# Performance work log

Measured on AMD Instinct MI355X. Metric: run time of the kernel, lower is better.

Reference implementation:

```python
import jax, jax.numpy as jnp
import numpy as np

N = 10000   # nodes
E = 320000  # edges
F = 512     # input features
H1 = 32
H2 = 16


def setup_inputs() -> dict:
    key = jax.random.key(0)
    k1, k2, k3, k4, k5, k6 = jax.random.split(key, 6)
    x = jax.random.normal(k1, (N, F), dtype=jnp.float32)
    edge_row = jax.random.randint(k2, (E,), 0, N, dtype=jnp.int32)
    edge_col = jax.random.randint(k3, (E,), 0, N, dtype=jnp.int32)
    edge_w = jax.random.uniform(k4, (E,), dtype=jnp.float32)  # normalized adj values
    W1 = jax.random.normal(k5, (F, H1), dtype=jnp.float32) * (1.0 / np.sqrt(F))
    W2 = jax.random.normal(k6, (H1, H2), dtype=jnp.float32) * (1.0 / np.sqrt(H1))
    return {"x": x, "edge_w": edge_w, "W1": W1, "W2": W2,
            "edge_row": edge_row, "edge_col": edge_col}


def _spmm(edge_w, edge_row, edge_col, h):
    # sparse A @ h : gather source rows, scale by edge weight, scatter-add to dest
    return jax.ops.segment_sum(edge_w[:, None] * h[edge_col], edge_row, num_segments=N)


def reference(x, edge_w, W1, W2, edge_row, edge_col):
    # GCN layer 1: relu(A @ (X W1))   (dropout rate 0 -> identity)
    h1 = jax.nn.relu(_spmm(edge_w, edge_row, edge_col, x @ W1))
    # GCN layer 2 (linear act): Z = A @ (H1 W2)
    z = _spmm(edge_w, edge_row, edge_col, h1 @ W2)
    # InnerProductDecoder: flatten(Z @ Z^T)
    recon = (z @ z.T).reshape(-1)
    return recon
```

## Files before the change

### kernel.cpp

```cpp
#include <hip/hip_runtime.h>


constexpr int N_   = 10000;
constexpr int E_   = 320000;
constexpr int F_   = 512;
constexpr int H1_  = 32;
constexpr int H2_  = 16;
constexpr int CAP_ = 96;

constexpr int GEMM_BLOCKS = (N_ * H1_) / 256;
constexpr int ZERO_BLOCKS = (N_ + 255) / 256;

__global__ __launch_bounds__(256) void gemm_xw1_zero(const float* __restrict__ x,
                                                     const float* __restrict__ W1,
                                                     float* __restrict__ h,
                                                     int* __restrict__ cursor) {
    if (blockIdx.x >= GEMM_BLOCKS) {
        int i = (blockIdx.x - GEMM_BLOCKS) * 256 + threadIdx.x;
        if (i < N_) cursor[i] = 0;
        return;
    }
    int tid = blockIdx.x * blockDim.x + threadIdx.x;
    int r = tid >> 5;
    int c = tid & (H1_ - 1);
    const float4* xr = reinterpret_cast<const float4*>(x + (size_t)r * F_);
    float acc = 0.f;
#pragma unroll 8
    for (int k4 = 0; k4 < F_ / 4; ++k4) {
        float4 xv = xr[k4];
        int k = k4 * 4;
        acc = fmaf(xv.x, W1[(k + 0) * H1_ + c], acc);
        acc = fmaf(xv.y, W1[(k + 1) * H1_ + c], acc);
        acc = fmaf(xv.z, W1[(k + 2) * H1_ + c], acc);
        acc = fmaf(xv.w, W1[(k + 3) * H1_ + c], acc);
    }
    h[tid] = acc;
}

__global__ __launch_bounds__(256) void scatter_ell(const int* __restrict__ erow,
                                                   const int* __restrict__ ecol,
                                                   const float* __restrict__ ew,
                                                   int* __restrict__ cursor,
                                                   int* __restrict__ cole,
                                                   float* __restrict__ we) {
    int e = blockIdx.x * blockDim.x + threadIdx.x;
    if (e >= E_) return;
    int r = erow[e];
    int p = atomicAdd(&cursor[r], 1);
    if (p < CAP_) {
        size_t idx = (size_t)r * CAP_ + p;
        cole[idx] = ecol[e];
        we[idx]   = ew[e];
    }
}

__global__ __launch_bounds__(256) void spmm1_mlp(const float* __restrict__ h,
                                                 const int* __restrict__ cursor,
                                                 const int* __restrict__ cole,
                                                 const float* __restrict__ we,
                                                 const float* __restrict__ W2,
                                                 float* __restrict__ h2) {
    __shared__ float sh1[8][H1_ + 1];
    __shared__ float sW2[H1_ * H2_];
    const int t = threadIdx.x;
    sW2[t]       = W2[t];
    sW2[t + 256] = W2[t + 256];

    const int rl = t >> 5;
    const int f  = t & (H1_ - 1);
    const int r  = blockIdx.x * 8 + rl;
    float acc = 0.f;
    if (r < N_) {
        const int deg = cursor[r];
        const int*   cp = cole + (size_t)r * CAP_;
        const float* wp = we   + (size_t)r * CAP_;
        int p = 0;
        for (; p + 4 <= deg; p += 4) {
            int c0 = cp[p], c1 = cp[p + 1], c2 = cp[p + 2], c3 = cp[p + 3];
            float w0 = wp[p], w1 = wp[p + 1], w2v = wp[p + 2], w3 = wp[p + 3];
            float g0 = h[(size_t)c0 * H1_ + f];
            float g1 = h[(size_t)c1 * H1_ + f];
            float g2 = h[(size_t)c2 * H1_ + f];
            float g3 = h[(size_t)c3 * H1_ + f];
            acc = fmaf(w0, g0, acc);
            acc = fmaf(w1, g1, acc);
            acc = fmaf(w2v, g2, acc);
            acc = fmaf(w3, g3, acc);
        }
        for (; p < deg; ++p)
            acc = fmaf(wp[p], h[(size_t)cp[p] * H1_ + f], acc);
    }
    sh1[rl][f] = fmaxf(acc, 0.f);
    __syncthreads();

    if (t < 128) {
        const int r2l = t >> 4;
        const int c   = t & (H2_ - 1);
        const int r2  = blockIdx.x * 8 + r2l;
        if (r2 < N_) {
            float a = 0.f;
#pragma unroll
            for (int k = 0; k < H1_; ++k)
                a = fmaf(sh1[r2l][k], sW2[k * H2_ + c], a);
            h2[(size_t)r2 * H2_ + c] = a;
        }
    }
}

__global__ __launch_bounds__(256) void spmm2(const float* __restrict__ h2,
                                             const int* __restrict__ cursor,
                                             const int* __restrict__ cole,
                                             const float* __restrict__ we,
                                             float* __restrict__ z) {
    const int t = threadIdx.x;
    const int rl = t >> 4;
    const int f  = t & (H2_ - 1);
    const int r  = blockIdx.x * 16 + rl;
    if (r >= N_) return;
    const int deg = cursor[r];
    const int*   cp = cole + (size_t)r * CAP_;
    const float* wp = we   + (size_t)r * CAP_;
    float acc = 0.f;
    int p = 0;
    for (; p + 4 <= deg; p += 4) {
        int c0 = cp[p], c1 = cp[p + 1], c2 = cp[p + 2], c3 = cp[p + 3];
        float w0 = wp[p], w1 = wp[p + 1], w2v = wp[p + 2], w3 = wp[p + 3];
        float g0 = h2[(size_t)c0 * H2_ + f];
        float g1 = h2[(size_t)c1 * H2_ + f];
        float g2 = h2[(size_t)c2 * H2_ + f];
        float g3 = h2[(size_t)c3 * H2_ + f];
        acc = fmaf(w0, g0, acc);
        acc = fmaf(w1, g1, acc);
        acc = fmaf(w2v, g2, acc);
        acc = fmaf(w3, g3, acc);
    }
    for (; p < deg; ++p)
        acc = fmaf(wp[p], h2[(size_t)cp[p] * H2_ + f], acc);
    z[(size_t)r * H2_ + f] = acc;
}

constexpr int BI = 32;
constexpr int BJ = 128;

__global__ __launch_bounds__(256) void zzt(const float* __restrict__ z,
                                           float* __restrict__ out) {
    __shared__ float zi[H2_][BI + 4];
    __shared__ float zj[H2_][BJ + 4];
    const int t  = threadIdx.x;
    const int ib = blockIdx.y * BI;
    const int jb = blockIdx.x * BJ;

    for (int idx = t; idx < BI * H2_; idx += 256) {
        int rl = idx >> 4;
        int k  = idx & 15;
        int gr = ib + rl;
        zi[k][rl] = (gr < N_) ? z[(size_t)gr * H2_ + k] : 0.f;
    }
    for (int idx = t; idx < BJ * H2_; idx += 256) {
        int rl = idx >> 4;
        int k  = idx & 15;
        int gr = jb + rl;
        zj[k][rl] = (gr < N_) ? z[(size_t)gr * H2_ + k] : 0.f;
    }
    __syncthreads();

    const int il = (t >> 5) << 2;
    const int jl = (t & 31) << 2;

    float acc[4][4] = {};
#pragma unroll
    for (int k = 0; k < H2_; ++k) {
        float4 a = *reinterpret_cast<const float4*>(&zi[k][il]);
        float4 b = *reinterpret_cast<const float4*>(&zj[k][jl]);
        acc[0][0] = fmaf(a.x, b.x, acc[0][0]);
        acc[0][1] = fmaf(a.x, b.y, acc[0][1]);
        acc[0][2] = fmaf(a.x, b.z, acc[0][2]);
        acc[0][3] = fmaf(a.x, b.w, acc[0][3]);
        acc[1][0] = fmaf(a.y, b.x, acc[1][0]);
        acc[1][1] = fmaf(a.y, b.y, acc[1][1]);
        acc[1][2] = fmaf(a.y, b.z, acc[1][2]);
        acc[1][3] = fmaf(a.y, b.w, acc[1][3]);
        acc[2][0] = fmaf(a.z, b.x, acc[2][0]);
        acc[2][1] = fmaf(a.z, b.y, acc[2][1]);
        acc[2][2] = fmaf(a.z, b.z, acc[2][2]);
        acc[2][3] = fmaf(a.z, b.w, acc[2][3]);
        acc[3][0] = fmaf(a.w, b.x, acc[3][0]);
        acc[3][1] = fmaf(a.w, b.y, acc[3][1]);
        acc[3][2] = fmaf(a.w, b.z, acc[3][2]);
        acc[3][3] = fmaf(a.w, b.w, acc[3][3]);
    }

#pragma unroll
    for (int ii = 0; ii < 4; ++ii) {
        int gi = ib + il + ii;
        if (gi >= N_) continue;
        int gj = jb + jl;
        float* orow = out + (size_t)gi * N_ + gj;
        if (gj + 3 < N_) {
            *reinterpret_cast<float4*>(orow) =
                make_float4(acc[ii][0], acc[ii][1], acc[ii][2], acc[ii][3]);
        } else {
#pragma unroll
            for (int jj = 0; jj < 4; ++jj)
                if (gj + jj < N_) orow[jj] = acc[ii][jj];
        }
    }
}

extern "C" void kernel_launch(void* const* d_in, const int* in_sizes, int n_in,
                              void* d_out, int out_size, void* d_ws, size_t ws_size,
                              hipStream_t stream) {
    const float* x    = (const float*)d_in[0];
    const float* ew   = (const float*)d_in[1];
    const float* W1   = (const float*)d_in[2];
    const float* W2   = (const float*)d_in[3];
    const int*   erow = (const int*)d_in[4];
    const int*   ecol = (const int*)d_in[5];
    float* out = (float*)d_out;

    float* h      = (float*)d_ws;
    float* h2     = h  + (size_t)N_ * H1_;
    float* z      = h2 + (size_t)N_ * H2_;
    float* we     = z  + (size_t)N_ * H2_;
    int*   cole   = (int*)(we + (size_t)N_ * CAP_);
    int*   cursor = cole + (size_t)N_ * CAP_;

    gemm_xw1_zero<<<GEMM_BLOCKS + ZERO_BLOCKS, 256, 0, stream>>>(x, W1, h, cursor);
    scatter_ell<<<(E_ + 255) / 256, 256, 0, stream>>>(erow, ecol, ew, cursor, cole, we);
    spmm1_mlp<<<(N_ + 7) / 8, 256, 0, stream>>>(h, cursor, cole, we, W2, h2);
    spmm2<<<(N_ + 15) / 16, 256, 0, stream>>>(h2, cursor, cole, we, z);

    dim3 grid((N_ + BJ - 1) / BJ, (N_ + BI - 1) / BI);
    zzt<<<grid, 256, 0, stream>>>(z, out);
}
```

Measured before the change: 216.1 us.

## Make ZZ^T blocks persistent over quarter-row strips, reusing the i-tile

```diff
diff --git a/kernel.cpp b/kernel.cpp
--- a/kernel.cpp
+++ b/kernel.cpp
@@ -139,70 +139,74 @@
     z[(size_t)r * H2_ + f] = acc;
 }
 
-constexpr int BI = 32;
-constexpr int BJ = 128;
-
-__global__ __launch_bounds__(256) void zzt(const float* __restrict__ z,
-                                           float* __restrict__ out) {
-    __shared__ float zi[H2_][BI + 4];
-    __shared__ float zj[H2_][BJ + 4];
+constexpr int ZBI = 32;
+constexpr int ZBJ = 128;
+constexpr int NQ  = 4;
+constexpr int QW  = N_ / NQ;
+constexpr int NSTRIP = (N_ + ZBI - 1) / ZBI;
+
+__global__ __launch_bounds__(256) void zzt_strip(const float* __restrict__ z,
+                                                 float* __restrict__ out) {
+    __shared__ float zi[H2_][ZBI + 4];
+    __shared__ float zj[H2_][ZBJ + 4];
     const int t  = threadIdx.x;
-    const int ib = blockIdx.y * BI;
-    const int jb = blockIdx.x * BJ;
-
-    for (int idx = t; idx < BI * H2_; idx += 256) {
-        int rl = idx >> 4;
-        int k  = idx & 15;
+    const int ib = (blockIdx.x >> 2) * ZBI;
+    const int jq = (blockIdx.x & 3) * QW;
+
+    for (int idx = t; idx < ZBI * H2_; idx += 256) {
+        int rl = idx >> 4, k = idx & 15;
         int gr = ib + rl;
         zi[k][rl] = (gr < N_) ? z[(size_t)gr * H2_ + k] : 0.f;
     }
-    for (int idx = t; idx < BJ * H2_; idx += 256) {
-        int rl = idx >> 4;
-        int k  = idx & 15;
-        int gr = jb + rl;
-        zj[k][rl] = (gr < N_) ? z[(size_t)gr * H2_ + k] : 0.f;
-    }
-    __syncthreads();
 
     const int il = (t >> 5) << 2;
     const int jl = (t & 31) << 2;
 
-    float acc[4][4] = {};
-#pragma unroll
-    for (int k = 0; k < H2_; ++k) {
-        float4 a = *reinterpret_cast<const float4*>(&zi[k][il]);
-        float4 b = *reinterpret_cast<const float4*>(&zj[k][jl]);
-        acc[0][0] = fmaf(a.x, b.x, acc[0][0]);
-        acc[0][1] = fmaf(a.x, b.y, acc[0][1]);
-        acc[0][2] = fmaf(a.x, b.z, acc[0][2]);
-        acc[0][3] = fmaf(a.x, b.w, acc[0][3]);
-        acc[1][0] = fmaf(a.y, b.x, acc[1][0]);
-        acc[1][1] = fmaf(a.y, b.y, acc[1][1]);
-        acc[1][2] = fmaf(a.y, b.z, acc[1][2]);
-        acc[1][3] = fmaf(a.y, b.w, acc[1][3]);
-        acc[2][0] = fmaf(a.z, b.x, acc[2][0]);
-        acc[2][1] = fmaf(a.z, b.y, acc[2][1]);
-        acc[2][2] = fmaf(a.z, b.z, acc[2][2]);
-        acc[2][3] = fmaf(a.z, b.w, acc[2][3]);
-        acc[3][0] = fmaf(a.w, b.x, acc[3][0]);
-        acc[3][1] = fmaf(a.w, b.y, acc[3][1]);
-        acc[3][2] = fmaf(a.w, b.z, acc[3][2]);
-        acc[3][3] = fmaf(a.w, b.w, acc[3][3]);
-    }
-
-#pragma unroll
-    for (int ii = 0; ii < 4; ++ii) {
-        int gi = ib + il + ii;
-        if (gi >= N_) continue;
-        int gj = jb + jl;
-        float* orow = out + (size_t)gi * N_ + gj;
-        if (gj + 3 < N_) {
-            *reinterpret_cast<float4*>(orow) =
-                make_float4(acc[ii][0], acc[ii][1], acc[ii][2], acc[ii][3]);
-        } else {
-#pragma unroll
-            for (int jj = 0; jj < 4; ++jj)
-                if (gj + jj < N_) orow[jj] = acc[ii][jj];
+    for (int cb = 0; cb < QW; cb += ZBJ) {
+        const int w = (QW - cb < ZBJ) ? (QW - cb) : ZBJ;
+        __syncthreads();
+        for (int idx = t; idx < ZBJ * H2_; idx += 256) {
+            int rl = idx >> 4, k = idx & 15;
+            zj[k][rl] = (rl < w) ? z[(size_t)(jq + cb + rl) * H2_ + k] : 0.f;
+        }
+        __syncthreads();
+
+        float acc[4][4] = {};
+#pragma unroll
+        for (int k = 0; k < H2_; ++k) {
+            float4 a = *reinterpret_cast<const float4*>(&zi[k][il]);
+            float4 b = *reinterpret_cast<const float4*>(&zj[k][jl]);
+            acc[0][0] = fmaf(a.x, b.x, acc[0][0]);
+            acc[0][1] = fmaf(a.x, b.y, acc[0][1]);
+            acc[0][2] = fmaf(a.x, b.z, acc[0][2]);
+            acc[0][3] = fmaf(a.x, b.w, acc[0][3]);
+            acc[1][0] = fmaf(a.y, b.x, acc[1][0]);
+            acc[1][1] = fmaf(a.y, b.y, acc[1][1]);
+            acc[1][2] = fmaf(a.y, b.z, acc[1][2]);
+            acc[1][3] = fmaf(a.y, b.w, acc[1][3]);
+            acc[2][0] = fmaf(a.z, b.x, acc[2][0]);
+            acc[2][1] = fmaf(a.z, b.y, acc[2][1]);
+            acc[2][2] = fmaf(a.z, b.z, acc[2][2]);
+            acc[2][3] = fmaf(a.z, b.w, acc[2][3]);
+            acc[3][0] = fmaf(a.w, b.x, acc[3][0]);
+            acc[3][1] = fmaf(a.w, b.y, acc[3][1]);
+            acc[3][2] = fmaf(a.w, b.z, acc[3][2]);
+            acc[3][3] = fmaf(a.w, b.w, acc[3][3]);
+        }
+
+        const int gjb = jq + cb + jl;
+#pragma unroll
+        for (int ii = 0; ii < 4; ++ii) {
+            int gi = ib + il + ii;
+            if (gi >= N_) continue;
+            if (jl + 3 < w) {
+                *reinterpret_cast<float4*>(out + (size_t)gi * N_ + gjb) =
+                    make_float4(acc[ii][0], acc[ii][1], acc[ii][2], acc[ii][3]);
+            } else {
+#pragma unroll
+                for (int jj = 0; jj < 4; ++jj)
+                    if (jl + jj < w) out[(size_t)gi * N_ + gjb + jj] = acc[ii][jj];
+            }
         }
     }
 }
@@ -230,6 +234,5 @@
     spmm1_mlp<<<(N_ + 7) / 8, 256, 0, stream>>>(h, cursor, cole, we, W2, h2);
     spmm2<<<(N_ + 15) / 16, 256, 0, stream>>>(h2, cursor, cole, we, z);
 
-    dim3 grid((N_ + BJ - 1) / BJ, (N_ + BI - 1) / BI);
-    zzt<<<grid, 256, 0, stream>>>(z, out);
-}
+    zzt_strip<<<NSTRIP * NQ, 256, 0, stream>>>(z, out);
+}
```

Result: slower. 288.4 us (+33.5%).

## Fuse front GCN stages into one cooperative kernel with grid syncs

Applied to the files above, without the earlier changes.

```diff
diff --git a/kernel.cpp b/kernel.cpp
--- a/kernel.cpp
+++ b/kernel.cpp
@@ -1,4 +1,7 @@
 #include <hip/hip_runtime.h>
+#include <hip/hip_cooperative_groups.h>
+
+namespace cg = cooperative_groups;
 
 
 constexpr int N_   = 10000;
@@ -8,135 +11,132 @@
 constexpr int H2_  = 16;
 constexpr int CAP_ = 96;
 
-constexpr int GEMM_BLOCKS = (N_ * H1_) / 256;
-constexpr int ZERO_BLOCKS = (N_ + 255) / 256;
-
-__global__ __launch_bounds__(256) void gemm_xw1_zero(const float* __restrict__ x,
-                                                     const float* __restrict__ W1,
-                                                     float* __restrict__ h,
-                                                     int* __restrict__ cursor) {
-    if (blockIdx.x >= GEMM_BLOCKS) {
-        int i = (blockIdx.x - GEMM_BLOCKS) * 256 + threadIdx.x;
-        if (i < N_) cursor[i] = 0;
-        return;
-    }
-    int tid = blockIdx.x * blockDim.x + threadIdx.x;
-    int r = tid >> 5;
-    int c = tid & (H1_ - 1);
-    const float4* xr = reinterpret_cast<const float4*>(x + (size_t)r * F_);
-    float acc = 0.f;
-#pragma unroll 8
-    for (int k4 = 0; k4 < F_ / 4; ++k4) {
-        float4 xv = xr[k4];
-        int k = k4 * 4;
-        acc = fmaf(xv.x, W1[(k + 0) * H1_ + c], acc);
-        acc = fmaf(xv.y, W1[(k + 1) * H1_ + c], acc);
-        acc = fmaf(xv.z, W1[(k + 2) * H1_ + c], acc);
-        acc = fmaf(xv.w, W1[(k + 3) * H1_ + c], acc);
-    }
-    h[tid] = acc;
-}
-
-__global__ __launch_bounds__(256) void scatter_ell(const int* __restrict__ erow,
+constexpr int COOP_BLOCKS = 1024;
+
+__global__ __launch_bounds__(256) void fused_front(const float* __restrict__ x,
+                                                   const float* __restrict__ W1,
+                                                   const float* __restrict__ W2,
+                                                   const float* __restrict__ ew,
+                                                   const int* __restrict__ erow,
                                                    const int* __restrict__ ecol,
-                                                   const float* __restrict__ ew,
+                                                   float* __restrict__ h,
+                                                   float* __restrict__ h2,
+                                                   float* __restrict__ z,
                                                    int* __restrict__ cursor,
                                                    int* __restrict__ cole,
                                                    float* __restrict__ we) {
-    int e = blockIdx.x * blockDim.x + threadIdx.x;
-    if (e >= E_) return;
-    int r = erow[e];
-    int p = atomicAdd(&cursor[r], 1);
-    if (p < CAP_) {
-        size_t idx = (size_t)r * CAP_ + p;
-        cole[idx] = ecol[e];
-        we[idx]   = ew[e];
-    }
-}
-
-__global__ __launch_bounds__(256) void spmm1_mlp(const float* __restrict__ h,
-                                                 const int* __restrict__ cursor,
-                                                 const int* __restrict__ cole,
-                                                 const float* __restrict__ we,
-                                                 const float* __restrict__ W2,
-                                                 float* __restrict__ h2) {
+    cg::grid_group grid = cg::this_grid();
+    const int t     = threadIdx.x;
+    const int gtid  = blockIdx.x * 256 + t;
+    const int gsize = gridDim.x * 256;
+
+    for (int i = gtid; i < N_; i += gsize) cursor[i] = 0;
+    for (int tid = gtid; tid < N_ * H1_; tid += gsize) {
+        int r = tid >> 5;
+        int c = tid & (H1_ - 1);
+        const float4* xr = reinterpret_cast<const float4*>(x + (size_t)r * F_);
+        float acc = 0.f;
+#pragma unroll 8
+        for (int k4 = 0; k4 < F_ / 4; ++k4) {
+            float4 xv = xr[k4];
+            int k = k4 * 4;
+            acc = fmaf(xv.x, W1[(k + 0) * H1_ + c], acc);
+            acc = fmaf(xv.y, W1[(k + 1) * H1_ + c], acc);
+            acc = fmaf(xv.z, W1[(k + 2) * H1_ + c], acc);
+            acc = fmaf(xv.w, W1[(k + 3) * H1_ + c], acc);
+        }
+        h[tid] = acc;
+    }
+    grid.sync();
+
+    for (int e = gtid; e < E_; e += gsize) {
+        int r = erow[e];
+        int p = atomicAdd(&cursor[r], 1);
+        if (p < CAP_) {
+            size_t idx = (size_t)r * CAP_ + p;
+            cole[idx] = ecol[e];
+            we[idx]   = ew[e];
+        }
+    }
+    grid.sync();
+
     __shared__ float sh1[8][H1_ + 1];
     __shared__ float sW2[H1_ * H2_];
-    const int t = threadIdx.x;
     sW2[t]       = W2[t];
     sW2[t + 256] = W2[t + 256];
-
-    const int rl = t >> 5;
-    const int f  = t & (H1_ - 1);
-    const int r  = blockIdx.x * 8 + rl;
-    float acc = 0.f;
-    if (r < N_) {
+    __syncthreads();
+
+    constexpr int NGROUP1 = (N_ + 7) / 8;
+    for (int g = blockIdx.x; g < NGROUP1; g += gridDim.x) {
+        __syncthreads();
+        const int rl = t >> 5;
+        const int f  = t & (H1_ - 1);
+        const int r  = g * 8 + rl;
+        float acc = 0.f;
+        if (r < N_) {
+            const int deg = cursor[r];
+            const int*   cp = cole + (size_t)r * CAP_;
+            const float* wp = we   + (size_t)r * CAP_;
+            int p = 0;
+            for (; p + 4 <= deg; p += 4) {
+                int c0 = cp[p], c1 = cp[p + 1], c2 = cp[p + 2], c3 = cp[p + 3];
+                float w0 = wp[p], w1 = wp[p + 1], w2v = wp[p + 2], w3 = wp[p + 3];
+                float g0 = h[(size_t)c0 * H1_ + f];
+                float g1 = h[(size_t)c1 * H1_ + f];
+                float g2 = h[(size_t)c2 * H1_ + f];
+                float g3 = h[(size_t)c3 * H1_ + f];
+                acc = fmaf(w0, g0, acc);
+                acc = fmaf(w1, g1, acc);
+                acc = fmaf(w2v, g2, acc);
+                acc = fmaf(w3, g3, acc);
+            }
+            for (; p < deg; ++p)
+                acc = fmaf(wp[p], h[(size_t)cp[p] * H1_ + f], acc);
+        }
+        sh1[rl][f] = fmaxf(acc, 0.f);
+        __syncthreads();
+        if (t < 128) {
+            const int r2l = t >> 4;
+            const int c   = t & (H2_ - 1);
+            const int r2  = g * 8 + r2l;
+            if (r2 < N_) {
+                float a = 0.f;
+#pragma unroll
+                for (int k = 0; k < H1_; ++k)
+                    a = fmaf(sh1[r2l][k], sW2[k * H2_ + c], a);
+                h2[(size_t)r2 * H2_ + c] = a;
+            }
+        }
+    }
+    grid.sync();
+
+    constexpr int NGROUP2 = (N_ + 15) / 16;
+    for (int g = blockIdx.x; g < NGROUP2; g += gridDim.x) {
+        const int rl = t >> 4;
+        const int f  = t & (H2_ - 1);
+        const int r  = g * 16 + rl;
+        if (r >= N_) continue;
         const int deg = cursor[r];
         const int*   cp = cole + (size_t)r * CAP_;
         const float* wp = we   + (size_t)r * CAP_;
+        float acc = 0.f;
         int p = 0;
         for (; p + 4 <= deg; p += 4) {
             int c0 = cp[p], c1 = cp[p + 1], c2 = cp[p + 2], c3 = cp[p + 3];
             float w0 = wp[p], w1 = wp[p + 1], w2v = wp[p + 2], w3 = wp[p + 3];
-            float g0 = h[(size_t)c0 * H1_ + f];
-            float g1 = h[(size_t)c1 * H1_ + f];
-            float g2 = h[(size_t)c2 * H1_ + f];
-            float g3 = h[(size_t)c3 * H1_ + f];
+            float g0 = h2[(size_t)c0 * H2_ + f];
+            float g1 = h2[(size_t)c1 * H2_ + f];
+            float g2 = h2[(size_t)c2 * H2_ + f];
+            float g3 = h2[(size_t)c3 * H2_ + f];
             acc = fmaf(w0, g0, acc);
             acc = fmaf(w1, g1, acc);
             acc = fmaf(w2v, g2, acc);
             acc = fmaf(w3, g3, acc);
         }
         for (; p < deg; ++p)
-            acc = fmaf(wp[p], h[(size_t)cp[p] * H1_ + f], acc);
-    }
-    sh1[rl][f] = fmaxf(acc, 0.f);
-    __syncthreads();
-
-    if (t < 128) {
-        const int r2l = t >> 4;
-        const int c   = t & (H2_ - 1);
-        const int r2  = blockIdx.x * 8 + r2l;
-        if (r2 < N_) {
-            float a = 0.f;
-#pragma unroll
-            for (int k = 0; k < H1_; ++k)
-                a = fmaf(sh1[r2l][k], sW2[k * H2_ + c], a);
-            h2[(size_t)r2 * H2_ + c] = a;
-        }
-    }
-}
-
-__global__ __launch_bounds__(256) void spmm2(const float* __restrict__ h2,
-                                             const int* __restrict__ cursor,
-                                             const int* __restrict__ cole,
-                                             const float* __restrict__ we,
-                                             float* __restrict__ z) {
-    const int t = threadIdx.x;
-    const int rl = t >> 4;
-    const int f  = t & (H2_ - 1);
-    const int r  = blockIdx.x * 16 + rl;
-    if (r >= N_) return;
-    const int deg = cursor[r];
-    const int*   cp = cole + (size_t)r * CAP_;
-    const float* wp = we   + (size_t)r * CAP_;
-    float acc = 0.f;
-    int p = 0;
-    for (; p + 4 <= deg; p += 4) {
-        int c0 = cp[p], c1 = cp[p + 1], c2 = cp[p + 2], c3 = cp[p + 3];
-        float w0 = wp[p], w1 = wp[p + 1], w2v = wp[p + 2], w3 = wp[p + 3];
-        float g0 = h2[(size_t)c0 * H2_ + f];
-        float g1 = h2[(size_t)c1 * H2_ + f];
-        float g2 = h2[(size_t)c2 * H2_ + f];
-        float g3 = h2[(size_t)c3 * H2_ + f];
-        acc = fmaf(w0, g0, acc);
-        acc = fmaf(w1, g1, acc);
-        acc = fmaf(w2v, g2, acc);
-        acc = fmaf(w3, g3, acc);
-    }
-    for (; p < deg; ++p)
-        acc = fmaf(wp[p], h2[(size_t)cp[p] * H2_ + f], acc);
-    z[(size_t)r * H2_ + f] = acc;
+            acc = fmaf(wp[p], h2[(size_t)cp[p] * H2_ + f], acc);
+        z[(size_t)r * H2_ + f] = acc;
+    }
 }
 
 constexpr int BI = 32;
@@ -225,10 +225,12 @@
     int*   cole   = (int*)(we + (size_t)N_ * CAP_);
     int*   cursor = cole + (size_t)N_ * CAP_;
 
-    gemm_xw1_zero<<<GEMM_BLOCKS + ZERO_BLOCKS, 256, 0, stream>>>(x, W1, h, cursor);
-    scatter_ell<<<(E_ + 255) / 256, 256, 0, stream>>>(erow, ecol, ew, cursor, cole, we);
-    spmm1_mlp<<<(N_ + 7) / 8, 256, 0, stream>>>(h, cursor, cole, we, W2, h2);
-    spmm2<<<(N_ + 15) / 16, 256, 0, stream>>>(h2, cursor, cole, we, z);
+    void* args[] = {(void*)&x, (void*)&W1, (void*)&W2, (void*)&ew,
+                    (void*)&erow, (void*)&ecol,
+                    (void*)&h, (void*)&h2, (void*)&z,
+                    (void*)&cursor, (void*)&cole, (void*)&we};
+    hipLaunchCooperativeKernel((const void*)fused_front, dim3(COOP_BLOCKS),
+                               dim3(256), args, 0, stream);
 
     dim3 grid((N_ + BJ - 1) / BJ, (N_ + BI - 1) / BI);
     zzt<<<grid, 256, 0, stream>>>(z, out);
```

Result: slower. 588.3 us (+172.2%).

## Enlarge ZZ^T tiles to 64x256, vectorize staging loads, use nontemporal output stores

Applied to the files above, without the earlier changes.

```diff
diff --git a/kernel.cpp b/kernel.cpp
--- a/kernel.cpp
+++ b/kernel.cpp
@@ -7,6 +7,8 @@
 constexpr int H1_  = 32;
 constexpr int H2_  = 16;
 constexpr int CAP_ = 96;
+
+typedef float f32x4 __attribute__((ext_vector_type(4)));
 
 constexpr int GEMM_BLOCKS = (N_ * H1_) / 256;
 constexpr int ZERO_BLOCKS = (N_ + 255) / 256;
@@ -139,70 +141,93 @@
     z[(size_t)r * H2_ + f] = acc;
 }
 
-constexpr int BI = 32;
-constexpr int BJ = 128;
+constexpr int BI = 64;
+constexpr int BJ = 256;
 
 __global__ __launch_bounds__(256) void zzt(const float* __restrict__ z,
                                            float* __restrict__ out) {
     __shared__ float zi[H2_][BI + 4];
-    __shared__ float zj[H2_][BJ + 4];
+    __shared__ float zj[H2_][BJ + 8];
     const int t  = threadIdx.x;
     const int ib = blockIdx.y * BI;
     const int jb = blockIdx.x * BJ;
 
-    for (int idx = t; idx < BI * H2_; idx += 256) {
-        int rl = idx >> 4;
-        int k  = idx & 15;
-        int gr = ib + rl;
-        zi[k][rl] = (gr < N_) ? z[(size_t)gr * H2_ + k] : 0.f;
-    }
-    for (int idx = t; idx < BJ * H2_; idx += 256) {
-        int rl = idx >> 4;
-        int k  = idx & 15;
-        int gr = jb + rl;
-        zj[k][rl] = (gr < N_) ? z[(size_t)gr * H2_ + k] : 0.f;
+    {
+        int row = t >> 2;
+        int kq  = (t & 3) * 4;
+        int gr  = ib + row;
+        float4 v = (gr < N_)
+            ? *reinterpret_cast<const float4*>(z + (size_t)gr * H2_ + kq)
+            : make_float4(0.f, 0.f, 0.f, 0.f);
+        zi[kq + 0][row] = v.x;
+        zi[kq + 1][row] = v.y;
+        zi[kq + 2][row] = v.z;
+        zi[kq + 3][row] = v.w;
+    }
+#pragma unroll
+    for (int it = 0; it < 4; ++it) {
+        int idx = it * 256 + t;
+        int row = idx >> 2;
+        int kq  = (idx & 3) * 4;
+        int gr  = jb + row;
+        float4 v = (gr < N_)
+            ? *reinterpret_cast<const float4*>(z + (size_t)gr * H2_ + kq)
+            : make_float4(0.f, 0.f, 0.f, 0.f);
+        zj[kq + 0][row] = v.x;
+        zj[kq + 1][row] = v.y;
+        zj[kq + 2][row] = v.z;
+        zj[kq + 3][row] = v.w;
     }
     __syncthreads();
 
-    const int il = (t >> 5) << 2;
-    const int jl = (t & 31) << 2;
-
-    float acc[4][4] = {};
+    const int tj = t & 31;
+    const int i0 = (t >> 5) * 8;
+
+    float4 accA[8] = {};
+    float4 accB[8] = {};
+
 #pragma unroll
     for (int k = 0; k < H2_; ++k) {
-        float4 a = *reinterpret_cast<const float4*>(&zi[k][il]);
-        float4 b = *reinterpret_cast<const float4*>(&zj[k][jl]);
-        acc[0][0] = fmaf(a.x, b.x, acc[0][0]);
-        acc[0][1] = fmaf(a.x, b.y, acc[0][1]);
-        acc[0][2] = fmaf(a.x, b.z, acc[0][2]);
-        acc[0][3] = fmaf(a.x, b.w, acc[0][3]);
-        acc[1][0] = fmaf(a.y, b.x, acc[1][0]);
-        acc[1][1] = fmaf(a.y, b.y, acc[1][1]);
-        acc[1][2] = fmaf(a.y, b.z, acc[1][2]);
-        acc[1][3] = fmaf(a.y, b.w, acc[1][3]);
-        acc[2][0] = fmaf(a.z, b.x, acc[2][0]);
-        acc[2][1] = fmaf(a.z, b.y, acc[2][1]);
-        acc[2][2] = fmaf(a.z, b.z, acc[2][2]);
-        acc[2][3] = fmaf(a.z, b.w, acc[2][3]);
-        acc[3][0] = fmaf(a.w, b.x, acc[3][0]);
-        acc[3][1] = fmaf(a.w, b.y, acc[3][1]);
-        acc[3][2] = fmaf(a.w, b.z, acc[3][2]);
-        acc[3][3] = fmaf(a.w, b.w, acc[3][3]);
-    }
-
-#pragma unroll
-    for (int ii = 0; ii < 4; ++ii) {
-        int gi = ib + il + ii;
-        if (gi >= N_) continue;
-        int gj = jb + jl;
-        float* orow = out + (size_t)gi * N_ + gj;
-        if (gj + 3 < N_) {
-            *reinterpret_cast<float4*>(orow) =
-                make_float4(acc[ii][0], acc[ii][1], acc[ii][2], acc[ii][3]);
+        float4 b0 = *reinterpret_cast<const float4*>(&zj[k][tj * 4]);
+        float4 b1 = *reinterpret_cast<const float4*>(&zj[k][128 + tj * 4]);
+        float4 a0 = *reinterpret_cast<const float4*>(&zi[k][i0]);
+        float4 a1 = *reinterpret_cast<const float4*>(&zi[k][i0 + 4]);
+        float av[8] = {a0.x, a0.y, a0.z, a0.w, a1.x, a1.y, a1.z, a1.w};
+#pragma unroll
+        for (int ii = 0; ii < 8; ++ii) {
+            accA[ii].x = fmaf(av[ii], b0.x, accA[ii].x);
+            accA[ii].y = fmaf(av[ii], b0.y, accA[ii].y);
+            accA[ii].z = fmaf(av[ii], b0.z, accA[ii].z);
+            accA[ii].w = fmaf(av[ii], b0.w, accA[ii].w);
+            accB[ii].x = fmaf(av[ii], b1.x, accB[ii].x);
+            accB[ii].y = fmaf(av[ii], b1.y, accB[ii].y);
+            accB[ii].z = fmaf(av[ii], b1.z, accB[ii].z);
+            accB[ii].w = fmaf(av[ii], b1.w, accB[ii].w);
+        }
+    }
+
+    const int j0 = jb + tj * 4;
+    const int j1 = jb + 128 + tj * 4;
+#pragma unroll
+    for (int ii = 0; ii < 8; ++ii) {
+        int gi = ib + i0 + ii;
+        if (gi >= N_) break;
+        float* orow = out + (size_t)gi * N_;
+        if (j0 + 3 < N_) {
+            f32x4 v = {accA[ii].x, accA[ii].y, accA[ii].z, accA[ii].w};
+            __builtin_nontemporal_store(v, reinterpret_cast<f32x4*>(orow + j0));
         } else {
-#pragma unroll
+            float a[4] = {accA[ii].x, accA[ii].y, accA[ii].z, accA[ii].w};
             for (int jj = 0; jj < 4; ++jj)
-                if (gj + jj < N_) orow[jj] = acc[ii][jj];
+                if (j0 + jj < N_) orow[j0 + jj] = a[jj];
+        }
+        if (j1 + 3 < N_) {
+            f32x4 v = {accB[ii].x, accB[ii].y, accB[ii].z, accB[ii].w};
+            __builtin_nontemporal_store(v, reinterpret_cast<f32x4*>(orow + j1));
+        } else {
+            float b[4] = {accB[ii].x, accB[ii].y, accB[ii].z, accB[ii].w};
+            for (int jj = 0; jj < 4; ++jj)
+                if (j1 + jj < N_) orow[j1 + jj] = b[jj];
         }
     }
 }
```

Measured after the change: 195.0 us. -9.8%, faster.
